# Performance work log

Measured on AMD Instinct MI355X. Metric: run time of the kernel, lower is better.

## Reference

```python
import jax, jax.numpy as jnp
import numpy as np

D_MODEL = 2048
NUM_HEADS = 16
HEAD_DIM = D_MODEL // NUM_HEADS
SCALE = HEAD_DIM ** 0.5
B, TQ, CACHE_LEN = 4, 1024, 1024


def setup_inputs() -> dict:
    key = jax.random.key(0)
    ks = jax.random.split(key, 13)
    f = jnp.float32
    inp = {
        'query': jax.random.normal(ks[0], (B, TQ, D_MODEL), f),
        'key': jax.random.normal(ks[1], (B, TQ, D_MODEL), f),
        'value': jax.random.normal(ks[2], (B, TQ, D_MODEL), f),
        'cache_key': jax.random.normal(ks[3], (B, CACHE_LEN, D_MODEL), f),
        'cache_value': jax.random.normal(ks[4], (B, CACHE_LEN, D_MODEL), f),
        'Wq': jax.random.normal(ks[5], (D_MODEL, D_MODEL), f) * 0.02,
        'bq': jnp.zeros((D_MODEL,), f),
        'Wk': jax.random.normal(ks[6], (D_MODEL, D_MODEL), f) * 0.02,
        'bk': jnp.zeros((D_MODEL,), f),
        'Wv': jax.random.normal(ks[7], (D_MODEL, D_MODEL), f) * 0.02,
        'bv': jnp.zeros((D_MODEL,), f),
        'Wo': jax.random.normal(ks[8], (D_MODEL, D_MODEL), f) * 0.02,
        'bo': jnp.zeros((D_MODEL,), f),
    }
    return inp


def _split(x):
    b, t, _ = x.shape
    return jnp.transpose(x.reshape(b, t, NUM_HEADS, HEAD_DIM), (0, 2, 1, 3))  # [B,H,T,Dh]


def reference(query, key, value, cache_key, cache_value, Wq, bq, Wk, bk, Wv, bv, Wo, bo):
    b, tq, _ = query.shape
    Q = query @ Wq.T + bq
    K = key @ Wk.T + bk
    V = value @ Wv.T + bv
    # cache holds already-projected K/V; concat along time
    K = jnp.concatenate([cache_key, K], axis=1)
    V = jnp.concatenate([cache_value, V], axis=1)
    total = K.shape[1]
    Qh, Kh, Vh = _split(Q), _split(K), _split(V)  # [B,H,T,Dh]
    scores = jnp.einsum('bhqd,bhkd->bhqk', Qh, Kh) / SCALE  # [B,H,Tq,total]
    # faithful to original: tril(Tq, total) mask (row i sees cols 0..i)
    mask = jnp.tril(jnp.ones((tq, total), dtype=bool))
    scores = jnp.where(mask[None, None], scores, -jnp.inf)
    attn = jax.nn.softmax(scores, axis=-1)  # eval mode: no dropout
    out = jnp.einsum('bhqk,bhkd->bhqd', attn, Vh)
    out = jnp.transpose(out, (0, 2, 1, 3)).reshape(b, tq, D_MODEL)
    out = out @ Wo.T + bo
    # new cache: torch reshapes the transposed [B,H,T,Dh] tensor directly
    new_k = Kh.reshape(b, -1, D_MODEL)
    new_v = Vh.reshape(b, -1, D_MODEL)
    return out, new_k, new_v
```

## Files before the change

### kernel.cpp

```cpp
#include <hip/hip_runtime.h>
#include <hip/hip_bf16.h>


typedef __bf16 bf16x8 __attribute__((ext_vector_type(8)));
typedef unsigned short u16x8 __attribute__((ext_vector_type(8)));
typedef float  f32x4  __attribute__((ext_vector_type(4)));
typedef unsigned int u32;

#define MFMA16(a, b, c) __builtin_amdgcn_mfma_f32_16x16x32_bf16((a), (b), (c), 0, 0, 0)

__device__ __forceinline__ void async16(__bf16* lds_p, const __bf16* g) {
    __builtin_amdgcn_global_load_lds(
        (__attribute__((address_space(1))) void*)g,
        (__attribute__((address_space(3))) void*)lds_p, 16, 0, 0);
}

__global__ __launch_bounds__(256) void prep(
    const float* __restrict__ q, const float* __restrict__ k, const float* __restrict__ v,
    const float* __restrict__ wq, const float* __restrict__ wk,
    const float* __restrict__ wv, const float* __restrict__ wo,
    const float* __restrict__ ck, const float* __restrict__ cv,
    float* __restrict__ nk, float* __restrict__ nv,
    __bf16* __restrict__ dq, __bf16* __restrict__ dk, __bf16* __restrict__ dv,
    __bf16* __restrict__ dwq, __bf16* __restrict__ dwk,
    __bf16* __restrict__ dwv, __bf16* __restrict__ dwo,
    __bf16* __restrict__ ckb, __bf16* __restrict__ cvb) {
    const int nthreads = gridDim.x * blockDim.x;
    for (int i = blockIdx.x * blockDim.x + threadIdx.x; i < 7340032; i += nthreads) {
        if (i < 2097152) {
            const int sel = i >> 20;
            const int j = i & 1048575;
            const int dh8 = j & 15;
            const int t = (j >> 4) & 1023;
            const int h = (j >> 14) & 15;
            const int b = j >> 18;
            const float* src = sel ? cv : ck;
            float* dst = sel ? nv : nk;
            __bf16* dstb = sel ? cvb : ckb;
            const size_t si = ((size_t)(b << 10) + t) * 2048 + (h << 7) + (dh8 << 3);
            const size_t di = ((size_t)b << 22) + ((size_t)h << 18) + (t << 7) + (dh8 << 3);
            const size_t bi = (((size_t)(b * 16 + h) * 1024 + t) << 7) + (dh8 << 3);
            const f32x4 x0 = *(const f32x4*)&src[si];
            const f32x4 x1 = *(const f32x4*)&src[si + 4];
            *(f32x4*)&dst[di] = x0;
            *(f32x4*)&dst[di + 4] = x1;
            bf16x8 bx;
#pragma unroll
            for (int e = 0; e < 4; e++) {
                bx[e]     = (__bf16)x0[e];
                bx[e + 4] = (__bf16)x1[e];
            }
            *(bf16x8*)&dstb[bi] = bx;
        } else {
            const float* s;
            __bf16* d;
            int off;
            if (i < 5242880) {
                const int ii = i - 2097152;
                const int r = ii >> 20;
                off = ii & 1048575;
                s = (r == 0) ? q : (r == 1) ? k : v;
                d = (r == 0) ? dq : (r == 1) ? dk : dv;
            } else {
                const int ii = i - 5242880;
                const int r = ii >> 19;
                off = ii & 524287;
                s = (r == 0) ? wq : (r == 1) ? wk : (r == 2) ? wv : wo;
                d = (r == 0) ? dwq : (r == 1) ? dwk : (r == 2) ? dwv : dwo;
            }
            const f32x4 x0 = *(const f32x4*)(s + (size_t)off * 8);
            const f32x4 x1 = *(const f32x4*)(s + (size_t)off * 8 + 4);
            bf16x8 o;
#pragma unroll
            for (int j2 = 0; j2 < 4; j2++) {
                o[j2]     = (__bf16)x0[j2];
                o[j2 + 4] = (__bf16)x1[j2];
            }
            *(bf16x8*)(d + (size_t)off * 8) = o;
        }
    }
}

template <int MODE>
__global__ __launch_bounds__(512, 2) void gemm8(
    const __bf16* __restrict__ A,
    const __bf16* __restrict__ W0, const __bf16* __restrict__ W1,
    const __bf16* __restrict__ W2,
    const float* __restrict__ bz0, const float* __restrict__ bz1,
    const float* __restrict__ bz2,
    void* __restrict__ C0, float* __restrict__ C1, float* __restrict__ C2) {
    extern __shared__ __bf16 lds[];
    constexpr int K = 2048;
    const int tid = threadIdx.x;
    const int w = tid >> 6, lane = tid & 63;
    const int wm = w >> 2, wn = w & 3;
    const int g = lane >> 4, c = lane & 15;

    const int lin = blockIdx.x;
    const int nb = lin & 7, mb = lin >> 3;
    const int m0 = mb << 7, n0 = nb << 8;
    const int seg = (MODE == 1) ? (mb >> 5) : 0;
    const __bf16* W = (MODE == 0 || seg == 0) ? W0 : (seg == 1) ? W1 : W2;
    const float* bias = (MODE == 0) ? bz0 : (seg == 0) ? bz0 : (seg == 1) ? bz1 : bz2;

    const __bf16* Ab = A + (size_t)m0 * K;
    const __bf16* Wb = W + (size_t)n0 * K;

    const int srow = lane >> 2;
    const int sch = (lane & 3) ^ (((lane >> 5) & 1) << 1);
    const int foff = c * 32 + ((g ^ ((c >> 3) << 1)) << 3);

    f32x4 acc[4][4] = {};

    auto stgA = [&](int T, int rg) {
#pragma unroll
        for (int u = 0; u < 2; u++) {
            const __bf16* gs = Ab + (size_t)(w * 16 + srow) * K + T * 64 + u * 32 + sch * 8;
            async16(&lds[rg * 24576 + (w * 2 + u) * 512], gs);
        }
    };
    auto stgB = [&](int T, int rg) {
#pragma unroll
        for (int u = 0; u < 4; u++) {
            const int rowblk = 2 * w + (u >> 1), kk = u & 1;
            const __bf16* gs = Wb + (size_t)(rowblk * 16 + srow) * K + T * 64 + kk * 32 + sch * 8;
            async16(&lds[rg * 24576 + 8192 + (w * 4 + u) * 512], gs);
        }
    };

    stgA(0, 0); stgB(0, 0);
    stgA(1, 1); stgB(1, 1);
    asm volatile("s_waitcnt vmcnt(6)" ::: "memory");
    asm volatile("s_barrier" ::: "memory");

    int rg = 0;
    for (int T = 0; T < 32; T++) {
        int rs = rg + 2; if (rs >= 3) rs -= 3;
        const int base = rg * 24576;
        bf16x8 fa[4], fb[4];

#pragma unroll
        for (int mi = 0; mi < 4; mi++)
            fa[mi] = *(const bf16x8*)&lds[base + ((wm * 4 + mi) * 2 + 0) * 512 + foff];
#pragma unroll
        for (int ni = 0; ni < 4; ni++)
            fb[ni] = *(const bf16x8*)&lds[base + 8192 + ((wn * 4 + ni) * 2 + 0) * 512 + foff];
        if (T < 30) stgA(T + 2, rs);
        asm volatile("s_barrier" ::: "memory");
        asm volatile("s_waitcnt lgkmcnt(0)" ::: "memory");
        __builtin_amdgcn_sched_barrier(0);
        __builtin_amdgcn_s_setprio(1);
#pragma unroll
        for (int mi = 0; mi < 4; mi++)
#pragma unroll
            for (int ni = 0; ni < 4; ni++)
                acc[mi][ni] = MFMA16(fa[mi], fb[ni], acc[mi][ni]);
        __builtin_amdgcn_s_setprio(0);
        asm volatile("s_barrier" ::: "memory");

#pragma unroll
        for (int mi = 0; mi < 4; mi++)
            fa[mi] = *(const bf16x8*)&lds[base + ((wm * 4 + mi) * 2 + 1) * 512 + foff];
#pragma unroll
        for (int ni = 0; ni < 4; ni++)
            fb[ni] = *(const bf16x8*)&lds[base + 8192 + ((wn * 4 + ni) * 2 + 1) * 512 + foff];
        if (T < 30) {
            stgB(T + 2, rs);
            asm volatile("s_waitcnt vmcnt(6)" ::: "memory");
        } else {
            asm volatile("s_waitcnt vmcnt(0)" ::: "memory");
        }
        asm volatile("s_barrier" ::: "memory");
        asm volatile("s_waitcnt lgkmcnt(0)" ::: "memory");
        __builtin_amdgcn_sched_barrier(0);
        __builtin_amdgcn_s_setprio(1);
#pragma unroll
        for (int mi = 0; mi < 4; mi++)
#pragma unroll
            for (int ni = 0; ni < 4; ni++)
                acc[mi][ni] = MFMA16(fa[mi], fb[ni], acc[mi][ni]);
        __builtin_amdgcn_s_setprio(0);
        asm volatile("s_barrier" ::: "memory");

        rg = (rg + 1 == 3) ? 0 : rg + 1;
    }

#pragma unroll
    for (int ni = 0; ni < 4; ni++) {
        const int col = n0 + wn * 64 + ni * 16 + c;
        const float bv = bias[col];
        const int h = col >> 7, dh = col & 127;
#pragma unroll
        for (int mi = 0; mi < 4; mi++) {
            const int rowb = m0 + wm * 64 + mi * 16 + g * 4;
#pragma unroll
            for (int r = 0; r < 4; r++) {
                const float v = acc[mi][ni][r] + bv;
                if (MODE == 0) {
                    ((float*)C0)[(size_t)(rowb + r) * 2048 + col] = v;
                } else {
                    const int lrow = (rowb + r) & 4095;
                    const int b = lrow >> 10, t = lrow & 1023;
                    if (seg == 0)
                        ((__bf16*)C0)[(((size_t)(b * 16 + h) * 1024) + t) * 128 + dh] = (__bf16)v;
                    else if (seg == 1)
                        C1[(((size_t)(b * 16 + h) * 2048) + 1024 + t) * 128 + dh] = v;
                    else
                        C2[(((size_t)(b * 16 + h) * 2048) + 1024 + t) * 128 + dh] = v;
                }
            }
        }
    }
}

__global__ __launch_bounds__(128) void attn_k(const __bf16* __restrict__ Qw,
                                              const __bf16* __restrict__ cK,
                                              const __bf16* __restrict__ cV,
                                              __bf16* __restrict__ O) {
    __shared__ __bf16 Kt[32 * 128];
    __shared__ u32 Vt32[128 * 16];
    __shared__ __bf16 Pw[2][16 * 32];

    const int tid = threadIdx.x;
    const int w = tid >> 6;
    const int lane = tid & 63;
    const int g = lane >> 4, c = lane & 15;

    const int lin = blockIdx.x + (blockIdx.y << 4) + (blockIdx.z << 8);
    const int xcd = lin & 7;
    const int j = lin >> 3;
    const int bh = xcd * 8 + (j & 7);
    const int qq = j >> 3;
    const int c4 = qq & 3, mq = qq >> 2;
    const int qb = ((mq & 1) == 0) ? (c4 * 4 + (mq >> 1)) : (31 - c4 * 4 - (mq >> 1));
    const int b = bh >> 4, h = bh & 15;
    const int q0 = qb << 5;
    const float inv_scale = 0.08838834764831845f;

    const __bf16* qbase = Qw + (((size_t)bh * 1024) + q0 + w * 16) * 128;
    bf16x8 qf[4];
#pragma unroll
    for (int dc = 0; dc < 4; dc++)
        qf[dc] = *(const bf16x8*)&qbase[c * 128 + dc * 32 + g * 8];

    f32x4 accO[8] = {};
    float m_run[4], l_run[4];
#pragma unroll
    for (int r = 0; r < 4; r++) { m_run[r] = -1e30f; l_run[r] = 0.0f; }

    const int trips = qb + 1;
    const __bf16* kb = cK + (size_t)bh * 1024 * 128;
    const __bf16* vb = cV + (size_t)bh * 1024 * 128;

    size_t ksrc[4];
    __bf16* kdst[4];
#pragma unroll
    for (int j2 = 0; j2 < 4; j2++) {
        const int keyb = w * 16 + j2 * 4;
        const int row = keyb + (lane >> 4);
        ksrc[j2] = (size_t)row * 128 + (((lane & 15) ^ (row & 7)) << 3);
        kdst[j2] = &Kt[keyb * 128];
    }

    const int kp = tid >> 3, dbv = tid & 7;
    const __bf16* vbase = vb + (size_t)(2 * kp) * 128 + dbv * 16;

    bf16x8 v0a = *(const bf16x8*)&vbase[0];
    bf16x8 v0b = *(const bf16x8*)&vbase[8];
    bf16x8 v1a = *(const bf16x8*)&vbase[128];
    bf16x8 v1b = *(const bf16x8*)&vbase[136];

    for (int kt = 0; kt < trips; kt++) {
        const int k0 = kt * 32;
        __syncthreads();
#pragma unroll
        for (int j2 = 0; j2 < 4; j2++)
            async16(kdst[j2], kb + (size_t)k0 * 128 + ksrc[j2]);
        {
            const u16x8 a0 = __builtin_bit_cast(u16x8, v0a);
            const u16x8 a1 = __builtin_bit_cast(u16x8, v0b);
            const u16x8 b0 = __builtin_bit_cast(u16x8, v1a);
            const u16x8 b1 = __builtin_bit_cast(u16x8, v1b);
#pragma unroll
            for (int jj = 0; jj < 8; jj++) {
                const int d0 = dbv * 16 + jj;
                const int d1 = d0 + 8;
                const int h0 = ((d0 >> 4) ^ (d0 >> 2)) & 3;
                const int h1 = ((d1 >> 4) ^ (d1 >> 2)) & 3;
                const int col0 = (((kp >> 2) ^ h0) << 2) | (kp & 3);
                const int col1 = (((kp >> 2) ^ h1) << 2) | (kp & 3);
                Vt32[d0 * 16 + col0] = (u32)a0[jj] | ((u32)b0[jj] << 16);
                Vt32[d1 * 16 + col1] = (u32)a1[jj] | ((u32)b1[jj] << 16);
            }
        }
        __syncthreads();

        const bool more = (kt + 1 < trips);
        bf16x8 n0a = {}, n0b = {}, n1a = {}, n1b = {};
        if (more) {
            const __bf16* vn = vbase + (size_t)(k0 + 32) * 128;
            n0a = *(const bf16x8*)&vn[0];
            n0b = *(const bf16x8*)&vn[8];
            n1a = *(const bf16x8*)&vn[128];
            n1b = *(const bf16x8*)&vn[136];
        }

        f32x4 s_acc[2] = {};
#pragma unroll
        for (int nt = 0; nt < 2; nt++) {
            const int krow = nt * 16 + c;
            const int ks = krow & 7;
#pragma unroll
            for (int dc = 0; dc < 4; dc++) {
                const bf16x8 kf =
                    *(const bf16x8*)&Kt[krow * 128 + (((dc * 4 + g) ^ ks) << 3)];
                s_acc[nt] = MFMA16(qf[dc], kf, s_acc[nt]);
            }
        }

        float p[2][4], alpha[4];
#pragma unroll
        for (int r = 0; r < 4; r++) {
            const int qrow = q0 + w * 16 + g * 4 + r;
            float s0 = (k0 + c      <= qrow) ? s_acc[0][r] * inv_scale : -1e30f;
            float s1 = (k0 + 16 + c <= qrow) ? s_acc[1][r] * inv_scale : -1e30f;
            float rm = fmaxf(s0, s1);
            rm = fmaxf(rm, __shfl_xor(rm, 1));
            rm = fmaxf(rm, __shfl_xor(rm, 2));
            rm = fmaxf(rm, __shfl_xor(rm, 4));
            rm = fmaxf(rm, __shfl_xor(rm, 8));
            const float mnew = fmaxf(m_run[r], rm);
            alpha[r] = __expf(m_run[r] - mnew);
            const float p0 = __expf(s0 - mnew);
            const float p1 = __expf(s1 - mnew);
            p[0][r] = p0; p[1][r] = p1;
            float ps = p0 + p1;
            ps += __shfl_xor(ps, 1);
            ps += __shfl_xor(ps, 2);
            ps += __shfl_xor(ps, 4);
            ps += __shfl_xor(ps, 8);
            l_run[r] = alpha[r] * l_run[r] + ps;
            m_run[r] = mnew;
        }
#pragma unroll
        for (int nt2 = 0; nt2 < 8; nt2++)
#pragma unroll
            for (int r = 0; r < 4; r++)
                accO[nt2][r] *= alpha[r];

#pragma unroll
        for (int nt = 0; nt < 2; nt++)
#pragma unroll
            for (int r = 0; r < 4; r++)
                Pw[w][(g * 4 + r) * 32 + ((((nt << 1) | (c >> 3)) ^ g) << 3) + (c & 7)] =
                    (__bf16)p[nt][r];
        asm volatile("s_waitcnt lgkmcnt(0)" ::: "memory");
        __builtin_amdgcn_sched_barrier(0);

        const bf16x8 pf = *(const bf16x8*)&Pw[w][c * 32 + ((g ^ ((c >> 2) & 3)) << 3)];
#pragma unroll
        for (int nt2 = 0; nt2 < 8; nt2++) {
            const int vrow = nt2 * 16 + c;
            const int hv = ((vrow >> 4) ^ (vrow >> 2)) & 3;
            const bf16x8 vf = *(const bf16x8*)&(
                (const __bf16*)Vt32)[vrow * 32 + ((g ^ hv) << 3)];
            accO[nt2] = MFMA16(pf, vf, accO[nt2]);
        }

        if (more) { v0a = n0a; v0b = n0b; v1a = n1a; v1b = n1b; }
    }

#pragma unroll
    for (int nt2 = 0; nt2 < 8; nt2++)
#pragma unroll
        for (int r = 0; r < 4; r++) {
            const float v = accO[nt2][r] / l_run[r];
            const int row = b * 1024 + q0 + w * 16 + g * 4 + r;
            const int col = h * 128 + nt2 * 16 + c;
            O[(size_t)row * 2048 + col] = (__bf16)v;
        }
}

extern "C" void kernel_launch(void* const* d_in, const int* in_sizes, int n_in,
                              void* d_out, int out_size, void* d_ws, size_t ws_size,
                              hipStream_t stream) {
    const float* query       = (const float*)d_in[0];
    const float* key         = (const float*)d_in[1];
    const float* value       = (const float*)d_in[2];
    const float* cache_key   = (const float*)d_in[3];
    const float* cache_value = (const float*)d_in[4];
    const float* Wq = (const float*)d_in[5];
    const float* bq = (const float*)d_in[6];
    const float* Wk = (const float*)d_in[7];
    const float* bk = (const float*)d_in[8];
    const float* Wv = (const float*)d_in[9];
    const float* bv = (const float*)d_in[10];
    const float* Wo = (const float*)d_in[11];
    const float* bo = (const float*)d_in[12];

    float* out   = (float*)d_out;
    float* new_k = out + 8388608;
    float* new_v = out + 25165824;

    __bf16* p = (__bf16*)d_ws;
    __bf16* ws_q    = p; p += 8388608;
    __bf16* ws_attn = p; p += 8388608;
    __bf16* q_bf    = p; p += 8388608;
    __bf16* k_bf    = p; p += 8388608;
    __bf16* v_bf    = p; p += 8388608;
    __bf16* wq_bf   = p; p += 4194304;
    __bf16* wk_bf   = p; p += 4194304;
    __bf16* wv_bf   = p; p += 4194304;
    __bf16* wo_bf   = p; p += 4194304;
    __bf16* ck_bf   = p; p += 8388608;
    __bf16* cv_bf   = p;

    static bool s_attr = false;
    if (!s_attr) {
        hipFuncSetAttribute(reinterpret_cast<const void*>(&gemm8<1>),
                            hipFuncAttributeMaxDynamicSharedMemorySize, 147456);
        hipFuncSetAttribute(reinterpret_cast<const void*>(&gemm8<0>),
                            hipFuncAttributeMaxDynamicSharedMemorySize, 147456);
        s_attr = true;
    }

    prep<<<4096, 256, 0, stream>>>(query, key, value, Wq, Wk, Wv, Wo,
                                   cache_key, cache_value, new_k, new_v,
                                   q_bf, k_bf, v_bf, wq_bf, wk_bf, wv_bf, wo_bf,
                                   ck_bf, cv_bf);
    gemm8<1><<<768, 512, 147456, stream>>>(q_bf, wq_bf, wk_bf, wv_bf,
                                           bq, bk, bv, ws_q, new_k, new_v);
    attn_k<<<dim3(16, 16, 8), 128, 0, stream>>>(ws_q, ck_bf, cv_bf, ws_attn);
    gemm8<0><<<256, 512, 147456, stream>>>(ws_attn, wo_bf, nullptr, nullptr,
                                           bo, nullptr, nullptr, out, nullptr, nullptr);
}
```

Before: 622.1 us.

## Move cache copy into QKV GEMM tail and add lazy softmax rescaling

The cache K/V transpose, copy and bf16 conversion move out of the prep kernel and run as a grid-stride epilogue of the fused QKV projection GEMM, so that memory-bound work can overlap with compute-bound blocks. The prep grid is halved to match its reduced work. In the attention kernel, the running max and output rescale are updated only when some row's max grows by more than 8 (checked wave-wide), which skips the per-tile multiply of the accumulator. Lazy rescaling relies on the fp32 accumulator tolerating exponentials up to e^8. The GEMM tail runs after each block's tile, which can lengthen the critical path of late blocks.

```diff
diff --git a/kernel.cpp b/kernel.cpp
--- a/kernel.cpp
+++ b/kernel.cpp
@@ -19,65 +19,35 @@
     const float* __restrict__ q, const float* __restrict__ k, const float* __restrict__ v,
     const float* __restrict__ wq, const float* __restrict__ wk,
     const float* __restrict__ wv, const float* __restrict__ wo,
-    const float* __restrict__ ck, const float* __restrict__ cv,
-    float* __restrict__ nk, float* __restrict__ nv,
     __bf16* __restrict__ dq, __bf16* __restrict__ dk, __bf16* __restrict__ dv,
     __bf16* __restrict__ dwq, __bf16* __restrict__ dwk,
-    __bf16* __restrict__ dwv, __bf16* __restrict__ dwo,
-    __bf16* __restrict__ ckb, __bf16* __restrict__ cvb) {
+    __bf16* __restrict__ dwv, __bf16* __restrict__ dwo) {
     const int nthreads = gridDim.x * blockDim.x;
-    for (int i = blockIdx.x * blockDim.x + threadIdx.x; i < 7340032; i += nthreads) {
-        if (i < 2097152) {
-            const int sel = i >> 20;
-            const int j = i & 1048575;
-            const int dh8 = j & 15;
-            const int t = (j >> 4) & 1023;
-            const int h = (j >> 14) & 15;
-            const int b = j >> 18;
-            const float* src = sel ? cv : ck;
-            float* dst = sel ? nv : nk;
-            __bf16* dstb = sel ? cvb : ckb;
-            const size_t si = ((size_t)(b << 10) + t) * 2048 + (h << 7) + (dh8 << 3);
-            const size_t di = ((size_t)b << 22) + ((size_t)h << 18) + (t << 7) + (dh8 << 3);
-            const size_t bi = (((size_t)(b * 16 + h) * 1024 + t) << 7) + (dh8 << 3);
-            const f32x4 x0 = *(const f32x4*)&src[si];
-            const f32x4 x1 = *(const f32x4*)&src[si + 4];
-            *(f32x4*)&dst[di] = x0;
-            *(f32x4*)&dst[di + 4] = x1;
-            bf16x8 bx;
-#pragma unroll
-            for (int e = 0; e < 4; e++) {
-                bx[e]     = (__bf16)x0[e];
-                bx[e + 4] = (__bf16)x1[e];
-            }
-            *(bf16x8*)&dstb[bi] = bx;
+    for (int i = blockIdx.x * blockDim.x + threadIdx.x; i < 5242880; i += nthreads) {
+        const float* s;
+        __bf16* d;
+        int off;
+        if (i < 3145728) {
+            const int r = i >> 20;
+            off = i & 1048575;
+            s = (r == 0) ? q : (r == 1) ? k : v;
+            d = (r == 0) ? dq : (r == 1) ? dk : dv;
         } else {
-            const float* s;
-            __bf16* d;
-            int off;
-            if (i < 5242880) {
-                const int ii = i - 2097152;
-                const int r = ii >> 20;
-                off = ii & 1048575;
-                s = (r == 0) ? q : (r == 1) ? k : v;
-                d = (r == 0) ? dq : (r == 1) ? dk : dv;
-            } else {
-                const int ii = i - 5242880;
-                const int r = ii >> 19;
-                off = ii & 524287;
-                s = (r == 0) ? wq : (r == 1) ? wk : (r == 2) ? wv : wo;
-                d = (r == 0) ? dwq : (r == 1) ? dwk : (r == 2) ? dwv : dwo;
-            }
-            const f32x4 x0 = *(const f32x4*)(s + (size_t)off * 8);
-            const f32x4 x1 = *(const f32x4*)(s + (size_t)off * 8 + 4);
-            bf16x8 o;
-#pragma unroll
-            for (int j2 = 0; j2 < 4; j2++) {
-                o[j2]     = (__bf16)x0[j2];
-                o[j2 + 4] = (__bf16)x1[j2];
-            }
-            *(bf16x8*)(d + (size_t)off * 8) = o;
-        }
+            const int ii = i - 3145728;
+            const int r = ii >> 19;
+            off = ii & 524287;
+            s = (r == 0) ? wq : (r == 1) ? wk : (r == 2) ? wv : wo;
+            d = (r == 0) ? dwq : (r == 1) ? dwk : (r == 2) ? dwv : dwo;
+        }
+        const f32x4 x0 = *(const f32x4*)(s + (size_t)off * 8);
+        const f32x4 x1 = *(const f32x4*)(s + (size_t)off * 8 + 4);
+        bf16x8 o;
+#pragma unroll
+        for (int j2 = 0; j2 < 4; j2++) {
+            o[j2]     = (__bf16)x0[j2];
+            o[j2 + 4] = (__bf16)x1[j2];
+        }
+        *(bf16x8*)(d + (size_t)off * 8) = o;
     }
 }
 
@@ -88,7 +58,10 @@
     const __bf16* __restrict__ W2,
     const float* __restrict__ bz0, const float* __restrict__ bz1,
     const float* __restrict__ bz2,
-    void* __restrict__ C0, float* __restrict__ C1, float* __restrict__ C2) {
+    void* __restrict__ C0, float* __restrict__ C1, float* __restrict__ C2,
+    const float* __restrict__ ck, const float* __restrict__ cv,
+    float* __restrict__ nkc, float* __restrict__ nvc,
+    __bf16* __restrict__ ckb, __bf16* __restrict__ cvb) {
     extern __shared__ __bf16 lds[];
     constexpr int K = 2048;
     const int tid = threadIdx.x;
@@ -211,6 +184,35 @@
             }
         }
     }
+
+    if (MODE == 1) {
+        const int nthr = gridDim.x * 512;
+        for (int i = blockIdx.x * 512 + tid; i < 2097152; i += nthr) {
+            const int sel = i >> 20;
+            const int j = i & 1048575;
+            const int dh8 = j & 15;
+            const int t = (j >> 4) & 1023;
+            const int h = (j >> 14) & 15;
+            const int b = j >> 18;
+            const float* src = sel ? cv : ck;
+            float* dst = sel ? nvc : nkc;
+            __bf16* dstb = sel ? cvb : ckb;
+            const size_t si = ((size_t)(b << 10) + t) * 2048 + (h << 7) + (dh8 << 3);
+            const size_t di = ((size_t)b << 22) + ((size_t)h << 18) + (t << 7) + (dh8 << 3);
+            const size_t bi = (((size_t)(b * 16 + h) * 1024 + t) << 7) + (dh8 << 3);
+            const f32x4 x0 = *(const f32x4*)&src[si];
+            const f32x4 x1 = *(const f32x4*)&src[si + 4];
+            *(f32x4*)&dst[di] = x0;
+            *(f32x4*)&dst[di + 4] = x1;
+            bf16x8 bx;
+#pragma unroll
+            for (int e = 0; e < 4; e++) {
+                bx[e]     = (__bf16)x0[e];
+                bx[e + 4] = (__bf16)x1[e];
+            }
+            *(bf16x8*)&dstb[bi] = bx;
+        }
+    }
 }
 
 __global__ __launch_bounds__(128) void attn_k(const __bf16* __restrict__ Qw,
@@ -318,21 +320,32 @@
             }
         }
 
-        float p[2][4], alpha[4];
+        float sv0[4], sv1[4], rmax[4];
 #pragma unroll
         for (int r = 0; r < 4; r++) {
             const int qrow = q0 + w * 16 + g * 4 + r;
-            float s0 = (k0 + c      <= qrow) ? s_acc[0][r] * inv_scale : -1e30f;
-            float s1 = (k0 + 16 + c <= qrow) ? s_acc[1][r] * inv_scale : -1e30f;
-            float rm = fmaxf(s0, s1);
+            sv0[r] = (k0 + c      <= qrow) ? s_acc[0][r] * inv_scale : -1e30f;
+            sv1[r] = (k0 + 16 + c <= qrow) ? s_acc[1][r] * inv_scale : -1e30f;
+            float rm = fmaxf(sv0[r], sv1[r]);
             rm = fmaxf(rm, __shfl_xor(rm, 1));
             rm = fmaxf(rm, __shfl_xor(rm, 2));
             rm = fmaxf(rm, __shfl_xor(rm, 4));
             rm = fmaxf(rm, __shfl_xor(rm, 8));
-            const float mnew = fmaxf(m_run[r], rm);
-            alpha[r] = __expf(m_run[r] - mnew);
-            const float p0 = __expf(s0 - mnew);
-            const float p1 = __expf(s1 - mnew);
+            rmax[r] = rm;
+        }
+        int grow = 0;
+#pragma unroll
+        for (int r = 0; r < 4; r++)
+            grow |= (rmax[r] > m_run[r] + 8.0f) ? 1 : 0;
+        const bool rescale = (bool)__any(grow);
+
+        float p[2][4], alpha[4];
+#pragma unroll
+        for (int r = 0; r < 4; r++) {
+            const float mnew = rescale ? fmaxf(m_run[r], rmax[r]) : m_run[r];
+            alpha[r] = rescale ? __expf(m_run[r] - mnew) : 1.0f;
+            const float p0 = __expf(sv0[r] - mnew);
+            const float p1 = __expf(sv1[r] - mnew);
             p[0][r] = p0; p[1][r] = p1;
             float ps = p0 + p1;
             ps += __shfl_xor(ps, 1);
@@ -342,11 +355,13 @@
             l_run[r] = alpha[r] * l_run[r] + ps;
             m_run[r] = mnew;
         }
-#pragma unroll
-        for (int nt2 = 0; nt2 < 8; nt2++)
-#pragma unroll
-            for (int r = 0; r < 4; r++)
-                accO[nt2][r] *= alpha[r];
+        if (rescale) {
+#pragma unroll
+            for (int nt2 = 0; nt2 < 8; nt2++)
+#pragma unroll
+                for (int r = 0; r < 4; r++)
+                    accO[nt2][r] *= alpha[r];
+        }
 
 #pragma unroll
         for (int nt = 0; nt < 2; nt++)
@@ -424,13 +439,15 @@
         s_attr = true;
     }
 
-    prep<<<4096, 256, 0, stream>>>(query, key, value, Wq, Wk, Wv, Wo,
-                                   cache_key, cache_value, new_k, new_v,
-                                   q_bf, k_bf, v_bf, wq_bf, wk_bf, wv_bf, wo_bf,
-                                   ck_bf, cv_bf);
+    prep<<<2048, 256, 0, stream>>>(query, key, value, Wq, Wk, Wv, Wo,
+                                   q_bf, k_bf, v_bf, wq_bf, wk_bf, wv_bf, wo_bf);
     gemm8<1><<<768, 512, 147456, stream>>>(q_bf, wq_bf, wk_bf, wv_bf,
-                                           bq, bk, bv, ws_q, new_k, new_v);
+                                           bq, bk, bv, ws_q, new_k, new_v,
+                                           cache_key, cache_value, new_k, new_v,
+                                           ck_bf, cv_bf);
     attn_k<<<dim3(16, 16, 8), 128, 0, stream>>>(ws_q, ck_bf, cv_bf, ws_attn);
     gemm8<0><<<256, 512, 147456, stream>>>(ws_attn, wo_bf, nullptr, nullptr,
-                                           bo, nullptr, nullptr, out, nullptr, nullptr);
+                                           bo, nullptr, nullptr, out, nullptr, nullptr,
+                                           nullptr, nullptr, nullptr, nullptr,
+                                           nullptr, nullptr);
 }
```

Result: no change. 626.6 us (+0.7%).
